# Kernel optimization log

Measured on AMD Instinct MI355X. Metric: run time of the kernel, lower is better.

Reference implementation:

```python
import jax, jax.numpy as jnp
import numpy as np

D_MODEL = 1024
NUM_HEADS = 16
D_K = D_MODEL // NUM_HEADS
MAX_REL = 128


def setup_inputs() -> dict:
    key = jax.random.key(0)
    ks = jax.random.split(key, 16)
    B, S = 4, 2048
    s = 1.0 / np.sqrt(D_MODEL)
    inp = {
        'query': jax.random.normal(ks[0], (B, S, D_MODEL), jnp.float32),
        'key': jax.random.normal(ks[1], (B, S, D_MODEL), jnp.float32),
        'value': jax.random.normal(ks[2], (B, S, D_MODEL), jnp.float32),
        'mask': jax.random.randint(ks[3], (B, 1, 1, S), 0, 2, jnp.int32),
        'Wq': jax.random.normal(ks[4], (D_MODEL, D_MODEL), jnp.float32) * s,
        'bq': jax.random.normal(ks[5], (D_MODEL,), jnp.float32) * 0.02,
        'Wk': jax.random.normal(ks[6], (D_MODEL, D_MODEL), jnp.float32) * s,
        'bk': jax.random.normal(ks[7], (D_MODEL,), jnp.float32) * 0.02,
        'Wv': jax.random.normal(ks[8], (D_MODEL, D_MODEL), jnp.float32) * s,
        'bv': jax.random.normal(ks[9], (D_MODEL,), jnp.float32) * 0.02,
        'Wo': jax.random.normal(ks[10], (D_MODEL, D_MODEL), jnp.float32) * s,
        'bo': jax.random.normal(ks[11], (D_MODEL,), jnp.float32) * 0.02,
        'rel_emb': jax.random.normal(ks[12], (2 * MAX_REL + 1, NUM_HEADS), jnp.float32) * 0.02,
    }
    return inp


def reference(query, key, value, mask, Wq, bq, Wk, bk, Wv, bv, Wo, bo, rel_emb):
    B, S, D = query.shape
    H, dk = NUM_HEADS, D_K
    # Linear projections (torch Linear: x @ W.T + b), split heads -> [B,H,S,dk]
    def proj(x, W, b):
        return (x @ W.T + b).reshape(B, S, H, dk).transpose(0, 2, 1, 3)
    Q = proj(query, Wq, bq)
    K = proj(key, Wk, bk)
    V = proj(value, Wv, bv)
    scores = jnp.einsum('bhqd,bhkd->bhqk', Q, K) / jnp.sqrt(jnp.float32(dk))
    # relative position bias: clamp(j-i, -M, M) + M, gather [S,S,H] -> [H,S,S]
    pos = jnp.arange(S)
    rel = jnp.clip(pos[None, :] - pos[:, None], -MAX_REL, MAX_REL) + MAX_REL
    bias = rel_emb[rel].transpose(2, 0, 1)  # [H,S,S]
    scores = scores + bias[None]
    scores = jnp.where(mask == 0, -jnp.inf, scores)
    weights = jax.nn.softmax(scores, axis=-1)
    weights = jnp.nan_to_num(weights, nan=0.0)  # fully-masked rows -> 0
    # dropout is identity in eval mode
    context = jnp.einsum('bhqk,bhkd->bhqd', weights, V)
    context = context.transpose(0, 2, 1, 3).reshape(B, S, D)
    return context @ Wo.T + bo
```

## Files before the change

### kernel.cpp

```cpp
#include <hip/hip_runtime.h>
#include <cstdint>
#include <cstddef>

typedef __bf16 bf16_t;
typedef __bf16 bf16x8 __attribute__((ext_vector_type(8)));
typedef float f32x4  __attribute__((ext_vector_type(4)));
typedef float f32x16 __attribute__((ext_vector_type(16)));
typedef int   i32x4  __attribute__((ext_vector_type(4)));

#define DEVI static __device__ __forceinline__

DEVI f32x4 mfma16(bf16x8 a, bf16x8 b, f32x4 c) {
  return __builtin_amdgcn_mfma_f32_16x16x32_bf16(a, b, c, 0, 0, 0);
}
DEVI f32x16 mfma32(bf16x8 a, bf16x8 b, f32x16 c) {
  return __builtin_amdgcn_mfma_f32_32x32x16_bf16(a, b, c, 0, 0, 0);
}
DEVI unsigned cvtpk(float lo, float hi) {
  unsigned d;
  asm("v_cvt_pk_bf16_f32 %0, %1, %2" : "=v"(d) : "v"(lo), "v"(hi));
  return d;
}
DEVI void gload_lds16(const bf16_t* g, bf16_t* l) {
  __builtin_amdgcn_global_load_lds(
      (const __attribute__((address_space(1))) void*)g,
      (__attribute__((address_space(3))) void*)l, 16, 0, 0);
}

#define L2E 1.44269504f
#define QSCALE (0.125f * L2E)

__global__ __launch_bounds__(256)
void cvt_qkv(const float* __restrict__ a0, const float* __restrict__ a1,
             const float* __restrict__ a2, bf16_t* __restrict__ o0,
             bf16_t* __restrict__ o1, bf16_t* __restrict__ o2, int n8)
{
  const int i = blockIdx.x * 256 + threadIdx.x;
  if (i >= n8) return;
  const float* in; bf16_t* out;
  if (blockIdx.y == 0)      { in = a0; out = o0; }
  else if (blockIdx.y == 1) { in = a1; out = o1; }
  else                      { in = a2; out = o2; }
  float4 a = ((const float4*)in)[2*i];
  float4 b = ((const float4*)in)[2*i + 1];
  bf16x8 o;
  o[0]=(bf16_t)a.x; o[1]=(bf16_t)a.y; o[2]=(bf16_t)a.z; o[3]=(bf16_t)a.w;
  o[4]=(bf16_t)b.x; o[5]=(bf16_t)b.y; o[6]=(bf16_t)b.z; o[7]=(bf16_t)b.w;
  ((bf16x8*)out)[i] = o;
}

__global__ __launch_bounds__(256)
void cvt_w(const float* __restrict__ wq, const float* __restrict__ wk,
           const float* __restrict__ wv, const float* __restrict__ wo,
           const int* __restrict__ mask,
           bf16_t* __restrict__ oq, bf16_t* __restrict__ ok,
           bf16_t* __restrict__ ov, bf16_t* __restrict__ ooh,
           bf16_t* __restrict__ ool, bf16_t* __restrict__ maskbit, int n8)
{
  const int i = blockIdx.x * 256 + threadIdx.x;
  const int y = blockIdx.y;
  if (y < 3) {
    if (i >= n8) return;
    const float* in = (y == 0) ? wq : (y == 1) ? wk : wv;
    bf16_t* out     = (y == 0) ? oq : (y == 1) ? ok : ov;
    float4 a = ((const float4*)in)[2*i];
    float4 b = ((const float4*)in)[2*i + 1];
    bf16x8 o;
    o[0]=(bf16_t)a.x; o[1]=(bf16_t)a.y; o[2]=(bf16_t)a.z; o[3]=(bf16_t)a.w;
    o[4]=(bf16_t)b.x; o[5]=(bf16_t)b.y; o[6]=(bf16_t)b.z; o[7]=(bf16_t)b.w;
    ((bf16x8*)out)[i] = o;
  } else if (y == 3) {
    if (i >= n8) return;
    float4 a = ((const float4*)wo)[2*i];
    float4 b = ((const float4*)wo)[2*i + 1];
    const float* f = (const float*)&a;
    bf16x8 oh, ol;
    #pragma unroll
    for (int j = 0; j < 4; ++j) { bf16_t h=(bf16_t)f[j]; oh[j]=h; ol[j]=(bf16_t)(f[j]-(float)h); }
    const float* f2 = (const float*)&b;
    #pragma unroll
    for (int j = 0; j < 4; ++j) { bf16_t h=(bf16_t)f2[j]; oh[4+j]=h; ol[4+j]=(bf16_t)(f2[j]-(float)h); }
    ((bf16x8*)ooh)[i] = oh;
    ((bf16x8*)ool)[i] = ol;
  } else {
    if (i >= 1024) return;
    i32x4 m0 = ((const i32x4*)mask)[2*i];
    i32x4 m1 = ((const i32x4*)mask)[2*i + 1];
    bf16x8 o;
    #pragma unroll
    for (int j = 0; j < 4; ++j) o[j]     = m0[j] ? (bf16_t)1.0f : (bf16_t)0.0f;
    #pragma unroll
    for (int j = 0; j < 4; ++j) o[4 + j] = m1[j] ? (bf16_t)1.0f : (bf16_t)0.0f;
    ((bf16x8*)maskbit)[i] = o;
  }
}

template<int OMODE>
__global__ __launch_bounds__(256)
void proj_gemm97(const bf16_t* __restrict__ A, const bf16_t* __restrict__ W,
                 const float* __restrict__ bias, bf16_t* __restrict__ Out,
                 float oscale, const int* __restrict__ mask)
{
  __shared__ __align__(16) bf16_t As[128 * 64];
  __shared__ __align__(16) bf16_t Bs[128 * 64];
  const int tid  = threadIdx.x;
  const int lane = tid & 63;
  const int w    = tid >> 6;
  const int g = lane >> 4, c = lane & 15;
  const int mq = (w >> 1) * 64, nq = (w & 1) * 64;
  const int bm = blockIdx.y, bn = blockIdx.x;

  const int rsub = lane >> 3;
  const int kc8  = (lane & 7) * 8;

  f32x4 acc[4][4] = {};

  for (int kt = 0; kt < 1024; kt += 64) {
    #pragma unroll
    for (int i = 0; i < 4; ++i) {
      const int inst = w * 4 + i;
      const int row  = inst * 8 + rsub;
      gload_lds16(A + (size_t)(bm*128 + row)*1024 + kt + kc8, &As[inst*512]);
      gload_lds16(W + (size_t)(bn*128 + row)*1024 + kt + kc8, &Bs[inst*512]);
    }
    __syncthreads();
    #pragma unroll
    for (int kk = 0; kk < 64; kk += 32) {
      bf16x8 af[4], bfv[4];
      #pragma unroll
      for (int i = 0; i < 4; ++i) {
        af[i]  = *(const bf16x8*)&As[(mq + i*16 + c)*64 + kk + 8*g];
        bfv[i] = *(const bf16x8*)&Bs[(nq + i*16 + c)*64 + kk + 8*g];
      }
      #pragma unroll
      for (int mi = 0; mi < 4; ++mi)
        #pragma unroll
        for (int ni = 0; ni < 4; ++ni)
          acc[mi][ni] = mfma16(af[mi], bfv[ni], acc[mi][ni]);
    }
    __syncthreads();
  }

  #pragma unroll
  for (int ni = 0; ni < 4; ++ni) {
    const int n = bn*128 + nq + ni*16 + c;
    const float bv = bias[n];
    const int h = n >> 6, d = n & 63;
    #pragma unroll
    for (int mi = 0; mi < 4; ++mi) {
      #pragma unroll
      for (int r = 0; r < 4; ++r) {
        const int m = bm*128 + mq + mi*16 + 4*g + r;
        const int bb = m >> 11, s = m & 2047;
        float v = (acc[mi][ni][r] + bv) * oscale;
        if (OMODE == 1) {
          Out[(((size_t)(bb*16 + h))*2048 + s)*64 + d] = (bf16_t)v;
        } else {
          if (mask[bb*2048 + s] == 0) v = 0.0f;
          Out[(((size_t)(bb*16 + h))*64 + d)*2048 + s] = (bf16_t)v;
        }
      }
    }
  }
}

__global__ __launch_bounds__(256)
void out_gemm97(const bf16_t* __restrict__ Ahg, const bf16_t* __restrict__ Alg,
                const bf16_t* __restrict__ Bhg, const bf16_t* __restrict__ Blg,
                const float* __restrict__ bias, float* __restrict__ Out)
{
  __shared__ __align__(16) bf16_t Ahs[128 * 64];
  __shared__ __align__(16) bf16_t Als[128 * 64];
  __shared__ __align__(16) bf16_t Bhs[128 * 64];
  __shared__ __align__(16) bf16_t Bls[128 * 64];
  const int tid  = threadIdx.x;
  const int lane = tid & 63;
  const int w    = tid >> 6;
  const int g = lane >> 4, c = lane & 15;
  const int mq = (w >> 1) * 64, nq = (w & 1) * 64;
  const int bm = blockIdx.y, bn = blockIdx.x;

  const int rsub = lane >> 3;
  const int kc8  = (lane & 7) * 8;

  f32x4 acc[4][4] = {};

  for (int kt = 0; kt < 1024; kt += 64) {
    #pragma unroll
    for (int i = 0; i < 4; ++i) {
      const int inst = w * 4 + i;
      const int row  = inst * 8 + rsub;
      const size_t ga = (size_t)(bm*128 + row)*1024 + kt + kc8;
      const size_t gb = (size_t)(bn*128 + row)*1024 + kt + kc8;
      gload_lds16(Ahg + ga, &Ahs[inst*512]);
      gload_lds16(Alg + ga, &Als[inst*512]);
      gload_lds16(Bhg + gb, &Bhs[inst*512]);
      gload_lds16(Blg + gb, &Bls[inst*512]);
    }
    __syncthreads();
    #pragma unroll
    for (int kk = 0; kk < 64; kk += 32) {
      bf16x8 afh[4], afl[4], bfh[4], bfl[4];
      #pragma unroll
      for (int i = 0; i < 4; ++i) {
        const int ar = (mq + i*16 + c)*64 + kk + 8*g;
        const int br = (nq + i*16 + c)*64 + kk + 8*g;
        afh[i] = *(const bf16x8*)&Ahs[ar];
        afl[i] = *(const bf16x8*)&Als[ar];
        bfh[i] = *(const bf16x8*)&Bhs[br];
        bfl[i] = *(const bf16x8*)&Bls[br];
      }
      #pragma unroll
      for (int mi = 0; mi < 4; ++mi)
        #pragma unroll
        for (int ni = 0; ni < 4; ++ni) {
          acc[mi][ni] = mfma16(afh[mi], bfh[ni], acc[mi][ni]);
          acc[mi][ni] = mfma16(afl[mi], bfh[ni], acc[mi][ni]);
          acc[mi][ni] = mfma16(afh[mi], bfl[ni], acc[mi][ni]);
        }
    }
    __syncthreads();
  }

  #pragma unroll
  for (int ni = 0; ni < 4; ++ni) {
    const int n = bn*128 + nq + ni*16 + c;
    const float bv = bias[n];
    #pragma unroll
    for (int mi = 0; mi < 4; ++mi)
      #pragma unroll
      for (int r = 0; r < 4; ++r) {
        const int m = bm*128 + mq + mi*16 + 4*g + r;
        Out[(size_t)m*1024 + n] = acc[mi][ni][r] + bv;
      }
  }
}

__global__ __launch_bounds__(256, 3)
void attn_kernel(const bf16_t* __restrict__ Q, const bf16_t* __restrict__ K,
                 const bf16_t* __restrict__ Vt, const bf16_t* __restrict__ maskbit,
                 const float* __restrict__ rel_emb,
                 bf16_t* __restrict__ Ch, bf16_t* __restrict__ Cl)
{
  __shared__ float relc[257];
  __shared__ __align__(16) bf16_t Ks[2][64][72];
  __shared__ __align__(16) bf16_t Vs[2][64][72];

  const int tid  = threadIdx.x;
  const int w    = tid >> 6;
  const int lane = tid & 63;
  const int lq   = lane & 31;
  const int hi   = lane >> 5;

  const int bid = blockIdx.x;
  const int n   = (bid & 7) * 128 + (bid >> 3);
  const int bh  = n >> 4;
  const int qblk= n & 15;
  const int b = bh >> 4, h = bh & 15;
  const int qw = qblk * 128 + w * 32;

  const bf16_t* Qb = Q  + ((size_t)bh * 2048) * 64;
  const bf16_t* Kb = K  + ((size_t)bh * 2048) * 64;
  const bf16_t* Vb = Vt + ((size_t)bh * 64) * 2048;
  const bf16_t* Mb = maskbit + (size_t)b * 2048;

  const int sr  = tid >> 2;
  const int so  = (tid & 3) * 16;

  for (int i = tid; i < 257; i += 256) relc[i] = rel_emb[i * 16 + h] * L2E;

  {
    const bf16_t* kp = Kb + (size_t)sr * 64 + so;
    const bf16_t* vp = Vb + (size_t)sr * 2048 + so;
    i32x4 k0 = *(const i32x4*)kp, k1 = *(const i32x4*)(kp + 8);
    i32x4 v0 = *(const i32x4*)vp, v1 = *(const i32x4*)(vp + 8);
    *(i32x4*)&Ks[0][sr][so] = k0;  *(i32x4*)&Ks[0][sr][so + 8] = k1;
    *(i32x4*)&Vs[0][sr][so] = v0;  *(i32x4*)&Vs[0][sr][so + 8] = v1;
  }
  __syncthreads();

  bf16x8 qf[4];
  #pragma unroll
  for (int dc = 0; dc < 4; ++dc)
    qf[dc] = *(const bf16x8*)&Qb[(size_t)(qw + lq) * 64 + dc * 16 + 8 * hi];

  const float biasLo = relc[0];
  const float biasHi = relc[256];

  f32x16 O0 = {}, O1 = {}, Ol = {};

  auto SMPK = [&](const f32x16& sa, int kvc, bf16x8& pa0, bf16x8& pa1) {
    unsigned u[8];
    const int d0 = kvc - qw;
    if (d0 >= 160 || d0 <= -160) {
      const float cb = (d0 >= 160) ? biasHi : biasLo;
      #pragma unroll
      for (int j = 0; j < 8; ++j)
        u[j] = cvtpk(exp2f(sa[2*j] + cb), exp2f(sa[2*j + 1] + cb));
    } else {
      #pragma unroll
      for (int j = 0; j < 8; ++j) {
        const int r0 = 2*j, r1 = 2*j + 1;
        const int k0r = (r0 & 3) + 8 * (r0 >> 2) + 4 * hi;
        const int k1r = (r1 & 3) + 8 * (r1 >> 2) + 4 * hi;
        int rr0 = kvc + k0r - (qw + lq);
        int rr1 = kvc + k1r - (qw + lq);
        rr0 = rr0 < -128 ? -128 : (rr0 > 128 ? 128 : rr0);
        rr1 = rr1 < -128 ? -128 : (rr1 > 128 ? 128 : rr1);
        u[j] = cvtpk(exp2f(sa[r0] + relc[rr0 + 128]),
                     exp2f(sa[r1] + relc[rr1 + 128]));
      }
    }
    asm volatile("v_permlane32_swap_b32 %0, %1" : "+v"(u[0]), "+v"(u[2]));
    asm volatile("v_permlane32_swap_b32 %0, %1" : "+v"(u[1]), "+v"(u[3]));
    i32x4 pw0 = { (int)u[0], (int)u[1], (int)u[2], (int)u[3] };
    pa0 = __builtin_bit_cast(bf16x8, pw0);
    asm volatile("v_permlane32_swap_b32 %0, %1" : "+v"(u[4]), "+v"(u[6]));
    asm volatile("v_permlane32_swap_b32 %0, %1" : "+v"(u[5]), "+v"(u[7]));
    i32x4 pw1 = { (int)u[4], (int)u[5], (int)u[6], (int)u[7] };
    pa1 = __builtin_bit_cast(bf16x8, pw1);
  };

  auto CHUNK = [&](int cur, int koff, int kvc) {
    bf16x8 kf[4];
    #pragma unroll
    for (int dc = 0; dc < 4; ++dc)
      kf[dc] = *(const bf16x8*)&Ks[cur][koff + lq][dc * 16 + 8 * hi];
    f32x16 sa = {};
    __builtin_amdgcn_s_setprio(1);
    #pragma unroll
    for (int dc = 0; dc < 4; ++dc) sa = mfma32(kf[dc], qf[dc], sa);
    __builtin_amdgcn_s_setprio(0);

    bf16x8 pa0, pa1;
    SMPK(sa, kvc, pa0, pa1);

    const int c0 = (koff >> 4) * 16;
    bf16x8 vf00 = *(const bf16x8*)&Vs[cur][lq]     [c0 + 8 * hi];
    bf16x8 vf01 = *(const bf16x8*)&Vs[cur][32 + lq][c0 + 8 * hi];
    bf16x8 vf10 = *(const bf16x8*)&Vs[cur][lq]     [c0 + 16 + 8 * hi];
    bf16x8 vf11 = *(const bf16x8*)&Vs[cur][32 + lq][c0 + 16 + 8 * hi];
    bf16x8 mba  = *(const bf16x8*)&Mb[kvc + 8 * hi];
    bf16x8 mbb  = *(const bf16x8*)&Mb[kvc + 16 + 8 * hi];
    __builtin_amdgcn_s_setprio(1);
    O0 = mfma32(pa0, vf00, O0);
    O1 = mfma32(pa0, vf01, O1);
    Ol = mfma32(pa0, mba,  Ol);
    O0 = mfma32(pa1, vf10, O0);
    O1 = mfma32(pa1, vf11, O1);
    Ol = mfma32(pa1, mbb,  Ol);
    __builtin_amdgcn_s_setprio(0);
  };

  for (int t = 0; t < 32; ++t) {
    const int kv  = t * 64;
    const int cur = t & 1, nxt = cur ^ 1;
    const bool more = (t + 1 < 32);

    i32x4 k0, k1, v0, v1;
    if (more) {
      const bf16_t* kp = Kb + (size_t)(kv + 64 + sr) * 64 + so;
      const bf16_t* vp = Vb + (size_t)sr * 2048 + (kv + 64) + so;
      k0 = *(const i32x4*)kp;  k1 = *(const i32x4*)(kp + 8);
      v0 = *(const i32x4*)vp;  v1 = *(const i32x4*)(vp + 8);
    }

    CHUNK(cur, 0, kv);

    if (more) {
      *(i32x4*)&Ks[nxt][sr][so] = k0;  *(i32x4*)&Ks[nxt][sr][so + 8] = k1;
      *(i32x4*)&Vs[nxt][sr][so] = v0;  *(i32x4*)&Vs[nxt][sr][so + 8] = v1;
    }

    CHUNK(cur, 32, kv + 32);

    __syncthreads();
  }

  #pragma unroll
  for (int reg = 0; reg < 16; ++reg) {
    const int qrow = (reg & 3) + 8 * (reg >> 2) + 4 * hi;
    const float sum = Ol[reg];
    const float iv = (sum > 0.0f) ? 1.0f / sum : 0.0f;
    const int s = qw + qrow;
    const size_t base = ((size_t)(b * 2048 + s)) * 1024 + h * 64 + lq;
    const float o0 = O0[reg] * iv, o1 = O1[reg] * iv;
    const bf16_t h0 = (bf16_t)o0, h1 = (bf16_t)o1;
    Ch[base]      = h0;  Cl[base]      = (bf16_t)(o0 - (float)h0);
    Ch[base + 32] = h1;  Cl[base + 32] = (bf16_t)(o1 - (float)h1);
  }
}

extern "C" void kernel_launch(void* const* d_in, const int* in_sizes, int n_in,
                              void* d_out, int out_size, void* d_ws, size_t ws_size,
                              hipStream_t stream)
{
  const float* q    = (const float*)d_in[0];
  const float* k    = (const float*)d_in[1];
  const float* v    = (const float*)d_in[2];
  const int*   mask = (const int*)  d_in[3];
  const float* Wq   = (const float*)d_in[4];
  const float* bq   = (const float*)d_in[5];
  const float* Wk   = (const float*)d_in[6];
  const float* bk   = (const float*)d_in[7];
  const float* Wv   = (const float*)d_in[8];
  const float* bv   = (const float*)d_in[9];
  const float* Wo   = (const float*)d_in[10];
  const float* bo   = (const float*)d_in[11];
  const float* rel  = (const float*)d_in[12];

  char* wsb = (char*)d_ws;
  bf16_t* Qw  = (bf16_t*)(wsb);
  bf16_t* Kw  = (bf16_t*)(wsb + ((size_t) 16 << 20));
  bf16_t* Vw  = (bf16_t*)(wsb + ((size_t) 32 << 20));
  bf16_t* Qc  = (bf16_t*)(wsb + ((size_t) 48 << 20));
  bf16_t* Kc  = (bf16_t*)(wsb + ((size_t) 64 << 20));
  bf16_t* Vc  = (bf16_t*)(wsb + ((size_t) 80 << 20));
  bf16_t* Wqc = (bf16_t*)(wsb + ((size_t) 96 << 20));
  bf16_t* Wkc = (bf16_t*)(wsb + ((size_t) 98 << 20));
  bf16_t* Wvc = (bf16_t*)(wsb + ((size_t)100 << 20));
  bf16_t* Woh = (bf16_t*)(wsb + ((size_t)102 << 20));
  bf16_t* Wol = (bf16_t*)(wsb + ((size_t)104 << 20));
  bf16_t* Mbit= (bf16_t*)(wsb + ((size_t)106 << 20));
  bf16_t* Chp = Qc;
  bf16_t* Clp = Kc;

  const int n8t = 8192 * 1024 / 8;
  const int n8w = 1024 * 1024 / 8;
  dim3 bb(256);

  cvt_qkv<<<dim3(4096, 3), bb, 0, stream>>>(q, k, v, Qc, Kc, Vc, n8t);
  cvt_w<<<dim3(512, 5), bb, 0, stream>>>(Wq, Wk, Wv, Wo, mask,
                                         Wqc, Wkc, Wvc, Woh, Wol, Mbit, n8w);

  dim3 gg(8, 64);
  proj_gemm97<1><<<gg, bb, 0, stream>>>(Qc, Wqc, bq, Qw, QSCALE, mask);
  proj_gemm97<1><<<gg, bb, 0, stream>>>(Kc, Wkc, bk, Kw, 1.0f, mask);
  proj_gemm97<2><<<gg, bb, 0, stream>>>(Vc, Wvc, bv, Vw, 1.0f, mask);
  attn_kernel<<<dim3(1024), bb, 0, stream>>>(Qw, Kw, Vw, Mbit, rel, Chp, Clp);
  out_gemm97<<<gg, bb, 0, stream>>>(Chp, Clp, Woh, Wol, bo, (float*)d_out);
}
```

Before: 283.0 us.

## Merge QKV projections into one launch and prefetch mask tiles in attention

The three projection GEMMs now run as a single launch with grid z selecting Q, K or V, so three 512-block launches become one 1536-block grid with better occupancy and fewer launch gaps. In the attention kernel, the mask fragments for the next KV tile are loaded into registers one iteration ahead (double-buffered in two register arrays, loop unrolled by two), and the V fragment loads are moved before the softmax packing to hide their latency. This adds register pressure in the attention kernel and makes the output mode a runtime branch rather than a template parameter.

```diff
diff --git a/kernel.cpp b/kernel.cpp
--- a/kernel.cpp
+++ b/kernel.cpp
@@ -95,14 +95,24 @@
   }
 }
 
-template<int OMODE>
 __global__ __launch_bounds__(256)
-void proj_gemm97(const bf16_t* __restrict__ A, const bf16_t* __restrict__ W,
-                 const float* __restrict__ bias, bf16_t* __restrict__ Out,
-                 float oscale, const int* __restrict__ mask)
+void proj_all(const bf16_t* __restrict__ Qc, const bf16_t* __restrict__ Kc,
+              const bf16_t* __restrict__ Vc, const bf16_t* __restrict__ Wqc,
+              const bf16_t* __restrict__ Wkc, const bf16_t* __restrict__ Wvc,
+              const float* __restrict__ bq, const float* __restrict__ bk,
+              const float* __restrict__ bv, bf16_t* __restrict__ Qw,
+              bf16_t* __restrict__ Kw, bf16_t* __restrict__ Vw,
+              const int* __restrict__ mask)
 {
   __shared__ __align__(16) bf16_t As[128 * 64];
   __shared__ __align__(16) bf16_t Bs[128 * 64];
+  const int z = blockIdx.z;
+  const bf16_t* A    = (z == 0) ? Qc  : (z == 1) ? Kc  : Vc;
+  const bf16_t* W    = (z == 0) ? Wqc : (z == 1) ? Wkc : Wvc;
+  const float*  bias = (z == 0) ? bq  : (z == 1) ? bk  : bv;
+  bf16_t*       Out  = (z == 0) ? Qw  : (z == 1) ? Kw  : Vw;
+  const float oscale = (z == 0) ? QSCALE : 1.0f;
+
   const int tid  = threadIdx.x;
   const int lane = tid & 63;
   const int w    = tid >> 6;
@@ -144,7 +154,7 @@
   #pragma unroll
   for (int ni = 0; ni < 4; ++ni) {
     const int n = bn*128 + nq + ni*16 + c;
-    const float bv = bias[n];
+    const float bv2 = bias[n];
     const int h = n >> 6, d = n & 63;
     #pragma unroll
     for (int mi = 0; mi < 4; ++mi) {
@@ -152,8 +162,8 @@
       for (int r = 0; r < 4; ++r) {
         const int m = bm*128 + mq + mi*16 + 4*g + r;
         const int bb = m >> 11, s = m & 2047;
-        float v = (acc[mi][ni][r] + bv) * oscale;
-        if (OMODE == 1) {
+        float v = (acc[mi][ni][r] + bv2) * oscale;
+        if (z != 2) {
           Out[(((size_t)(bb*16 + h))*2048 + s)*64 + d] = (bf16_t)v;
         } else {
           if (mask[bb*2048 + s] == 0) v = 0.0f;
@@ -269,6 +279,7 @@
 
   for (int i = tid; i < 257; i += 256) relc[i] = rel_emb[i * 16 + h] * L2E;
 
+  bf16x8 mb0[4], mb1[4];
   {
     const bf16_t* kp = Kb + (size_t)sr * 64 + so;
     const bf16_t* vp = Vb + (size_t)sr * 2048 + so;
@@ -276,6 +287,9 @@
     i32x4 v0 = *(const i32x4*)vp, v1 = *(const i32x4*)(vp + 8);
     *(i32x4*)&Ks[0][sr][so] = k0;  *(i32x4*)&Ks[0][sr][so + 8] = k1;
     *(i32x4*)&Vs[0][sr][so] = v0;  *(i32x4*)&Vs[0][sr][so + 8] = v1;
+    #pragma unroll
+    for (int j = 0; j < 4; ++j)
+      mb0[j] = *(const bf16x8*)&Mb[j * 16 + 8 * hi];
   }
   __syncthreads();
 
@@ -321,7 +335,7 @@
     pa1 = __builtin_bit_cast(bf16x8, pw1);
   };
 
-  auto CHUNK = [&](int cur, int koff, int kvc) {
+  auto CHUNK = [&](int cur, int koff, int kvc, bf16x8 mba, bf16x8 mbb) {
     bf16x8 kf[4];
     #pragma unroll
     for (int dc = 0; dc < 4; ++dc)
@@ -332,16 +346,15 @@
     for (int dc = 0; dc < 4; ++dc) sa = mfma32(kf[dc], qf[dc], sa);
     __builtin_amdgcn_s_setprio(0);
 
-    bf16x8 pa0, pa1;
-    SMPK(sa, kvc, pa0, pa1);
-
-    const int c0 = (koff >> 4) * 16;
+    const int c0 = koff;
     bf16x8 vf00 = *(const bf16x8*)&Vs[cur][lq]     [c0 + 8 * hi];
     bf16x8 vf01 = *(const bf16x8*)&Vs[cur][32 + lq][c0 + 8 * hi];
     bf16x8 vf10 = *(const bf16x8*)&Vs[cur][lq]     [c0 + 16 + 8 * hi];
     bf16x8 vf11 = *(const bf16x8*)&Vs[cur][32 + lq][c0 + 16 + 8 * hi];
-    bf16x8 mba  = *(const bf16x8*)&Mb[kvc + 8 * hi];
-    bf16x8 mbb  = *(const bf16x8*)&Mb[kvc + 16 + 8 * hi];
+
+    bf16x8 pa0, pa1;
+    SMPK(sa, kvc, pa0, pa1);
+
     __builtin_amdgcn_s_setprio(1);
     O0 = mfma32(pa0, vf00, O0);
     O1 = mfma32(pa0, vf01, O1);
@@ -352,9 +365,9 @@
     __builtin_amdgcn_s_setprio(0);
   };
 
-  for (int t = 0; t < 32; ++t) {
+  auto ITER = [&](int t, int cur, bf16x8 (&mbc)[4], bf16x8 (&mbn)[4]) {
     const int kv  = t * 64;
-    const int cur = t & 1, nxt = cur ^ 1;
+    const int nxt = cur ^ 1;
     const bool more = (t + 1 < 32);
 
     i32x4 k0, k1, v0, v1;
@@ -363,18 +376,27 @@
       const bf16_t* vp = Vb + (size_t)sr * 2048 + (kv + 64) + so;
       k0 = *(const i32x4*)kp;  k1 = *(const i32x4*)(kp + 8);
       v0 = *(const i32x4*)vp;  v1 = *(const i32x4*)(vp + 8);
-    }
-
-    CHUNK(cur, 0, kv);
+      #pragma unroll
+      for (int j = 0; j < 4; ++j)
+        mbn[j] = *(const bf16x8*)&Mb[kv + 64 + j * 16 + 8 * hi];
+    }
+
+    CHUNK(cur, 0, kv, mbc[0], mbc[1]);
 
     if (more) {
       *(i32x4*)&Ks[nxt][sr][so] = k0;  *(i32x4*)&Ks[nxt][sr][so + 8] = k1;
       *(i32x4*)&Vs[nxt][sr][so] = v0;  *(i32x4*)&Vs[nxt][sr][so + 8] = v1;
     }
 
-    CHUNK(cur, 32, kv + 32);
+    CHUNK(cur, 32, kv + 32, mbc[2], mbc[3]);
 
     __syncthreads();
+  };
+
+  #pragma unroll 1
+  for (int t = 0; t < 32; t += 2) {
+    ITER(t,     0, mb0, mb1);
+    ITER(t + 1, 1, mb1, mb0);
   }
 
   #pragma unroll
@@ -433,10 +455,8 @@
   cvt_w<<<dim3(512, 5), bb, 0, stream>>>(Wq, Wk, Wv, Wo, mask,
                                          Wqc, Wkc, Wvc, Woh, Wol, Mbit, n8w);
 
-  dim3 gg(8, 64);
-  proj_gemm97<1><<<gg, bb, 0, stream>>>(Qc, Wqc, bq, Qw, QSCALE, mask);
-  proj_gemm97<1><<<gg, bb, 0, stream>>>(Kc, Wkc, bk, Kw, 1.0f, mask);
-  proj_gemm97<2><<<gg, bb, 0, stream>>>(Vc, Wvc, bv, Vw, 1.0f, mask);
+  proj_all<<<dim3(8, 64, 3), bb, 0, stream>>>(Qc, Kc, Vc, Wqc, Wkc, Wvc,
+                                              bq, bk, bv, Qw, Kw, Vw, mask);
   attn_kernel<<<dim3(1024), bb, 0, stream>>>(Qw, Kw, Vw, Mbit, rel, Chp, Clp);
-  out_gemm97<<<gg, bb, 0, stream>>>(Chp, Clp, Woh, Wol, bo, (float*)d_out);
-}
+  out_gemm97<<<dim3(8, 64), bb, 0, stream>>>(Chp, Clp, Woh, Wol, bo, (float*)d_out);
+}
```

After: 308.3 us. 1.09x slower.
